# Kernel optimization log

Measured on AMD Instinct MI355X. Metric: run time of the kernel, lower is better.

The kernel has to match this reference:

```python
import jax, jax.numpy as jnp
import numpy as np

N = 8192
IN_DIM = 512
OUT_DIM = 512


def setup_inputs() -> dict:
    key = jax.random.key(0)
    kA, kX, k1, k2, k3, k4 = jax.random.split(key, 6)
    A = jax.random.uniform(kA, (N, N), dtype=jnp.float32)  # strictly positive -> nonzero triu
    X = jax.random.normal(kX, (N, IN_DIM), dtype=jnp.float32)
    s = 1.0 / np.sqrt(IN_DIM)
    W1 = jax.random.uniform(k1, (OUT_DIM, IN_DIM), minval=-s, maxval=s, dtype=jnp.float32)  # fc
    b1 = jax.random.uniform(k2, (OUT_DIM,), minval=-s, maxval=s, dtype=jnp.float32)
    W2 = jax.random.uniform(k3, (OUT_DIM, IN_DIM), minval=-s, maxval=s, dtype=jnp.float32)  # fc2
    b2 = jax.random.uniform(k4, (OUT_DIM,), minval=-s, maxval=s, dtype=jnp.float32)
    return {"A": A, "X": X, "W1": W1, "b1": b1, "W2": W2, "b2": b2}


def reference(A, X, W1, b1, W2, b2):
    n = A.shape[0]
    # strictly upper-triangular mask (diagonal=1); with uniform(0,1) fill all these
    # entries are nonzero, so torch.nonzero selects exactly them: m = n(n-1)/2 values.
    triu_mask = jnp.triu(jnp.ones((n, n), dtype=bool), k=1)
    m = n * (n - 1) // 2
    # torch.median = lower median = sorted[(m-1)//2]; pad non-triu entries with +inf
    vals = jnp.where(triu_mask, A, jnp.inf).reshape(-1)
    median_value = jnp.sort(vals)[(m - 1) // 2]
    # A[A < median] = 0
    A_thr = jnp.where(A < median_value, jnp.zeros((), A.dtype), A)
    A_norm = jax.nn.softmax(A_thr, axis=-1)
    fcX = X @ W1.T + b1    # [N, out_dim]
    fc2X = X @ W2.T + b2   # [N, out_dim]
    out = jax.nn.leaky_relu(0.1 * fc2X + 0.9 * (A_norm @ fcX), negative_slope=0.01)
    return out
```

## Files before the change

### kernel.cpp

```cpp
#include <hip/hip_runtime.h>

#define DEVI __device__ __forceinline__

typedef __attribute__((ext_vector_type(8))) short short8;
typedef __attribute__((ext_vector_type(4))) float f32x4;

static constexpr int NN = 8192;
static constexpr int DD = 512;
static constexpr unsigned LOB = 0x3EFE0000u;
static constexpr unsigned HIB = 0x3F020000u;
static constexpr long long K_RANK = 16775167LL;

static constexpr size_t WS_HIST = 0;
static constexpr size_t WS_CNT  = 1048576;
static constexpr size_t WS_MED  = 1048832;
static constexpr size_t WS_XB   = 2097152;
static constexpr size_t WS_W1B  = WS_XB  + (size_t)NN * DD * 2;
static constexpr size_t WS_W2B  = WS_W1B + (size_t)DD * DD * 2;
static constexpr size_t WS_FCXT = WS_W2B + (size_t)DD * DD * 2;
static constexpr size_t WS_FC2  = WS_FCXT + (size_t)NN * DD * 2;
static constexpr size_t WS_UP   = WS_FC2 + (size_t)NN * DD * 4;
static constexpr size_t WS_ZP   = WS_UP  + (size_t)4 * NN * DD * 2;

DEVI unsigned short f2bf(float f) {
  unsigned u = __float_as_uint(f);
  u += 0x7fffu + ((u >> 16) & 1u);
  return (unsigned short)(u >> 16);
}
DEVI float bf2f(unsigned short h) { return __uint_as_float(((unsigned)h) << 16); }
DEVI int swz(int row, int kq) { return kq ^ ((row >> 1) & 3); }

DEVI void gl_lds16(const void* g, void* l) {
  __builtin_amdgcn_global_load_lds(
      (const __attribute__((address_space(1))) unsigned*)g,
      (__attribute__((address_space(3))) unsigned*)l, 16, 0, 0);
}

#define VMCNT(n) asm volatile("s_waitcnt vmcnt(" #n ")" ::: "memory")
#define LGKM0 asm volatile("s_waitcnt lgkmcnt(0)" ::: "memory")


DEVI void convert_body(const float* __restrict__ X, const float* __restrict__ W1,
                       const float* __restrict__ W2, unsigned short* __restrict__ Xb,
                       unsigned short* __restrict__ W1b, unsigned short* __restrict__ W2b,
                       int cb, int tid) {
  const long long NX = (long long)NN * DD;
  const long long NW = (long long)DD * DD;
  const long long total4 = (NX + 2 * NW) / 4;
  for (long long q = (long long)cb * 512 + tid; q < total4; q += 65536LL) {
    long long e = q << 2;
    const float4* src; unsigned short* dst; long long off;
    if (e < NX)           { src = (const float4*)X;  dst = Xb;  off = e; }
    else if (e < NX + NW) { src = (const float4*)W1; dst = W1b; off = e - NX; }
    else                  { src = (const float4*)W2; dst = W2b; off = e - NX - NW; }
    float4 v = src[off >> 2];
    ushort4 o;
    o.x = f2bf(v.x); o.y = f2bf(v.y); o.z = f2bf(v.z); o.w = f2bf(v.w);
    *(ushort4*)(dst + off) = o;
  }
}

DEVI void hist_body(const float* __restrict__ A, unsigned* __restrict__ hist,
                    unsigned* __restrict__ below, int hb, int tid) {
  unsigned cnt = 0;
  const float4* A4 = (const float4*)A;
  for (long long q = (long long)hb * 512 + tid; q < 16777216LL; q += 458752LL) {
    long long base = q << 2;
    int row = (int)(base >> 13);
    int col = (int)(base & 8191);
    if (col + 3 <= row) continue;
    float4 v = A4[q];
    float vv[4] = {v.x, v.y, v.z, v.w};
#pragma unroll
    for (int j = 0; j < 4; ++j) {
      if (col + j > row) {
        unsigned u = __float_as_uint(vv[j]);
        if (u < LOB) cnt++;
        else if (u < HIB) atomicAdd(&hist[u - LOB], 1u);
      }
    }
  }
  for (int off = 32; off > 0; off >>= 1) cnt += __shfl_down(cnt, off);
  if ((tid & 63) == 0 && cnt) atomicAdd(below, cnt);
}

__global__ __launch_bounds__(512) void stage1_k(const float* __restrict__ A,
                                                const float* __restrict__ X,
                                                const float* __restrict__ W1,
                                                const float* __restrict__ W2,
                                                unsigned* __restrict__ hist,
                                                unsigned* __restrict__ below,
                                                unsigned short* __restrict__ Xb,
                                                unsigned short* __restrict__ W1b,
                                                unsigned short* __restrict__ W2b) {
  const int bx = blockIdx.x;
  if (bx < 128) convert_body(X, W1, W2, Xb, W1b, W2b, bx, threadIdx.x);
  else          hist_body(A, hist, below, bx - 128, threadIdx.x);
}


template <bool BROW, bool OBF>
DEVI void gemm_small_body(const unsigned short* __restrict__ Am,
                          const unsigned short* __restrict__ Bm,
                          const float* __restrict__ bias, void* __restrict__ outp,
                          int ldout, int m0, int n0, char* apB, char* btB) {
  const int tid = threadIdx.x, lane = tid & 63, w = tid >> 6;
  const int wm = w >> 2, wn = w & 3;
  const int lr = lane & 15, lq = lane >> 4;
  const int rL = lane >> 2, kq = lane & 3;
  f32x4 acc[2][4];
#pragma unroll
  for (int i = 0; i < 2; ++i)
#pragma unroll
    for (int j = 0; j < 4; ++j) acc[i][j] = (f32x4){0.f, 0.f, 0.f, 0.f};

#pragma unroll 1
  for (int kt = 0; kt < 16; ++kt) {
    const int k0 = kt * 32;
    __syncthreads();
    if (w < 4) {
      int r = w * 16 + rL;
      gl_lds16(Am + ((size_t)(m0 + r) * DD + k0 + swz(r, kq) * 8), apB + w * 1024);
    }
#pragma unroll
    for (int i = 0; i < 2; ++i) {
      int blk = w * 2 + i;
      int r = blk * 16 + rL;
      gl_lds16(Bm + ((size_t)(n0 + r) * DD + k0 + swz(r, kq) * 8), btB + blk * 1024);
    }
    __syncthreads();
    short8 a[2], b[4];
#pragma unroll
    for (int fr = 0; fr < 2; ++fr) {
      int r = wm * 32 + fr * 16 + lr;
      a[fr] = *(const short8*)(apB + r * 64 + swz(r, lq) * 16);
    }
#pragma unroll
    for (int fc = 0; fc < 4; ++fc) {
      int r = wn * 64 + fc * 16 + lr;
      b[fc] = *(const short8*)(btB + r * 64 + swz(r, lq) * 16);
    }
#pragma unroll
    for (int fr = 0; fr < 2; ++fr)
#pragma unroll
      for (int fc = 0; fc < 4; ++fc)
        acc[fr][fc] = __builtin_amdgcn_mfma_f32_16x16x32_bf16(a[fr], b[fc], acc[fr][fc], 0, 0, 0);
  }
#pragma unroll
  for (int fr = 0; fr < 2; ++fr)
#pragma unroll
    for (int fc = 0; fc < 4; ++fc)
#pragma unroll
      for (int j = 0; j < 4; ++j) {
        int row = m0 + wm * 32 + fr * 16 + lq * 4 + j;
        int col = n0 + wn * 64 + fc * 16 + lr;
        float v = acc[fr][fc][j] + (BROW ? bias[row] : bias[col]);
        if (OBF) ((unsigned short*)outp)[(size_t)row * ldout + col] = f2bf(v);
        else     ((float*)outp)[(size_t)row * ldout + col] = v;
      }
}

__global__ __launch_bounds__(512, 2) void stage2_k(const unsigned short* __restrict__ Xb,
                                                   const unsigned short* __restrict__ W1b,
                                                   const unsigned short* __restrict__ W2b,
                                                   const float* __restrict__ b1,
                                                   const float* __restrict__ b2,
                                                   unsigned short* __restrict__ fcXT,
                                                   float* __restrict__ fc2) {
  __shared__ alignas(16) char plds[20480];
  const int bx = blockIdx.x;
  if (bx < 256) {
    int m0 = ((bx >> 3) & 7) * 64;
    int n0 = ((bx & 7) | ((bx >> 6) << 3)) * 256;
    gemm_small_body<true, true>(W1b, Xb, b1, (void*)fcXT, NN, m0, n0, plds, plds + 4096);
  } else {
    int q = bx - 256;
    gemm_small_body<false, false>(Xb, W2b, b2, (void*)fc2, DD,
                                  (q >> 1) * 64, (q & 1) * 256, plds, plds + 4096);
  }
}

__global__ __launch_bounds__(1024) void select_k(const unsigned* __restrict__ hist,
                                                 const unsigned* __restrict__ below,
                                                 unsigned* __restrict__ med) {
  __shared__ unsigned ssum[1024];
  __shared__ int owner;
  __shared__ unsigned tg_s;
  const int t = threadIdx.x;
  unsigned own = 0;
  const uint4* h4 = (const uint4*)(hist + t * 256);
#pragma unroll 8
  for (int b = 0; b < 64; ++b) {
    uint4 v = h4[b];
    own += v.x + v.y + v.z + v.w;
  }
  ssum[t] = own;
  __syncthreads();
  for (int off = 1; off < 1024; off <<= 1) {
    unsigned v = (t >= off) ? ssum[t - off] : 0u;
    __syncthreads();
    ssum[t] += v;
    __syncthreads();
  }
  long long target = K_RANK - (long long)(*below);
  unsigned incl = ssum[t];
  unsigned excl = incl - own;
  if (target >= (long long)excl && target < (long long)incl) {
    owner = t;
    tg_s = (unsigned)(target - (long long)excl);
  }
  __syncthreads();
  const int to = owner;
  const unsigned tg = tg_s;
  unsigned v256 = (t < 256) ? hist[to * 256 + t] : 0u;
  __syncthreads();
  if (t < 256) ssum[t] = v256;
  __syncthreads();
  for (int off = 1; off < 256; off <<= 1) {
    unsigned v = (t < 256 && t >= off) ? ssum[t - off] : 0u;
    __syncthreads();
    if (t < 256) ssum[t] += v;
    __syncthreads();
  }
  if (t < 256) {
    unsigned incl2 = ssum[t];
    unsigned excl2 = incl2 - v256;
    if (tg >= excl2 && tg < incl2) *med = LOB + (unsigned)(to * 256 + t);
  }
}

static constexpr int LDS_A0 = 0;
static constexpr int LDS_A1 = 8192;
static constexpr int LDS_B0 = 16384;
static constexpr int LDS_B1 = 49152;

__global__ __launch_bounds__(512, 2) void main_gemm_k(const float* __restrict__ A,
                                                      const unsigned short* __restrict__ fcXT,
                                                      const unsigned* __restrict__ medp,
                                                      unsigned short* __restrict__ Up,
                                                      float* __restrict__ Zp) {
  __shared__ alignas(16) char lds[81920];
  const int tid = threadIdx.x, lane = tid & 63, w = tid >> 6;
  const int wm = w >> 2, wn = w & 3;
  const int lr = lane & 15, lq = lane >> 4;
  const int fid = blockIdx.x;
  const int xcd = fid & 7;
  const int ks = xcd >> 1;
  const int m0 = (((xcd & 1) << 5) | (fid >> 3)) << 7;
  const int kbase = ks * 2048;
  const float med = __uint_as_float(*medp);
  const int rB = lane >> 2, kqB = lane & 3;
  const int rA = tid >> 2, cqA = tid & 3;
  const float* aRow = A + (size_t)(m0 + rA) * NN;
  const int ldsAw = rA * 64 + swz(rA, cqA) * 16;

  float zacc = 0.f;
  f32x4 acc[4][8];
#pragma unroll
  for (int i = 0; i < 4; ++i)
#pragma unroll
    for (int j = 0; j < 8; ++j) acc[i][j] = (f32x4){0.f, 0.f, 0.f, 0.f};
  float4 vA00, vA01, vA10, vA11;

#define CONV8(V0, V1, DST)                                                     \
  {                                                                            \
    float vv[8] = {V0.x, V0.y, V0.z, V0.w, V1.x, V1.y, V1.z, V1.w};            \
    short8 pb;                                                                 \
    _Pragma("unroll")                                                          \
    for (int j = 0; j < 8; ++j) {                                              \
      float a_ = vv[j];                                                        \
      float p_ = (a_ < med) ? 1.0f : __expf(a_);                               \
      unsigned short h_ = f2bf(p_);                                            \
      pb[j] = (short)h_;                                                       \
      zacc += bf2f(h_);                                                        \
    }                                                                          \
    *(short8*)(DST) = pb;                                                      \
  }

  {
#pragma unroll
    for (int i = 0; i < 4; ++i) {
      int blk = w * 4 + i;
      int o = blk * 16 + rB;
      gl_lds16(fcXT + ((size_t)o * NN + kbase + swz(o, kqB) * 8), lds + LDS_B0 + blk * 1024);
    }
    const float* ap0 = aRow + kbase + cqA * 8;
    float4 t0 = *(const float4*)ap0;
    float4 t1 = *(const float4*)(ap0 + 4);
    vA00 = *(const float4*)(ap0 + 32);
    vA01 = *(const float4*)(ap0 + 36);
    CONV8(t0, t1, lds + LDS_A0 + ldsAw);
  }
  __syncthreads();

#define ITER(KT, CUR, NCUR, VAC0, VAC1, VAN0, VAN1)                            \
  {                                                                            \
    const int kt_ = (KT);                                                      \
    if (kt_ < 63) {                                                            \
      const int k1 = kbase + (kt_ + 1) * 32;                                   \
      _Pragma("unroll")                                                        \
      for (int i = 0; i < 4; ++i) {                                            \
        int blk = w * 4 + i;                                                   \
        int o = blk * 16 + rB;                                                 \
        gl_lds16(fcXT + ((size_t)o * NN + k1 + swz(o, kqB) * 8),               \
                 lds + LDS_B##NCUR + blk * 1024);                              \
      }                                                                        \
      if (kt_ < 62) {                                                          \
        const float* apf = aRow + kbase + (kt_ + 2) * 32 + cqA * 8;            \
        asm volatile("global_load_dwordx4 %0, %2, off\n\t"                     \
                     "global_load_dwordx4 %1, %2, off offset:16"               \
                     : "=&v"(VAN0), "=&v"(VAN1)                                \
                     : "v"(apf)                                                \
                     : "memory");                                              \
      }                                                                        \
    }                                                                          \
    short8 af[4], bfr[8];                                                      \
    _Pragma("unroll")                                                          \
    for (int fr = 0; fr < 4; ++fr) {                                           \
      int r = wm * 64 + fr * 16 + lr;                                          \
      af[fr] = *(const short8*)(lds + LDS_A##CUR + r * 64 + swz(r, lq) * 16);  \
    }                                                                          \
    _Pragma("unroll")                                                          \
    for (int fc = 0; fc < 8; ++fc) {                                           \
      int o = wn * 128 + fc * 16 + lr;                                         \
      bfr[fc] = *(const short8*)(lds + LDS_B##CUR + o * 64 + swz(o, lq) * 16); \
    }                                                                          \
    __builtin_amdgcn_s_setprio(1);                                             \
    _Pragma("unroll")                                                          \
    for (int fr = 0; fr < 4; ++fr)                                             \
      _Pragma("unroll")                                                        \
      for (int fc = 0; fc < 8; ++fc)                                           \
        acc[fr][fc] = __builtin_amdgcn_mfma_f32_16x16x32_bf16(af[fr], bfr[fc], \
                                                              acc[fr][fc], 0, 0, 0); \
    __builtin_amdgcn_s_setprio(0);                                             \
    if (kt_ < 63) {                                                            \
      if (kt_ < 62) { VMCNT(6); } else { VMCNT(4); }                           \
      __builtin_amdgcn_sched_barrier(0);                                       \
      CONV8(VAC0, VAC1, lds + LDS_A##NCUR + ldsAw);                            \
      if (kt_ < 62) { VMCNT(2); } else { VMCNT(0); }                           \
      LGKM0;                                                                   \
      __builtin_amdgcn_s_barrier();                                            \
    }                                                                          \
  }

#pragma unroll 1
  for (int t2 = 0; t2 < 32; ++t2) {
    ITER(2 * t2,     0, 1, vA00, vA01, vA10, vA11);
    ITER(2 * t2 + 1, 1, 0, vA10, vA11, vA00, vA01);
  }
#undef ITER
#undef CONV8

  zacc += __shfl_xor(zacc, 1);
  zacc += __shfl_xor(zacc, 2);
  if ((lane & 3) == 0) Zp[(size_t)ks * NN + m0 + rA] = zacc;
#pragma unroll
  for (int fr = 0; fr < 4; ++fr)
#pragma unroll
    for (int fc = 0; fc < 8; ++fc)
#pragma unroll
      for (int j = 0; j < 4; ++j) {
        int row = m0 + wm * 64 + fr * 16 + lq * 4 + j;
        int col = wn * 128 + fc * 16 + lr;
        Up[((size_t)ks << 22) + ((size_t)row << 9) + col] = f2bf(acc[fr][fc][j]);
      }
}

__global__ __launch_bounds__(256) void reduce_k(const unsigned short* __restrict__ Up,
                                                const float* __restrict__ Zp,
                                                const float* __restrict__ fc2,
                                                float* __restrict__ out) {
  long long t = (long long)blockIdx.x * blockDim.x + threadIdx.x;
  if (t >= (long long)NN * DD / 8) return;
  long long base = t << 3;
  int row = (int)(base >> 9);
  float Z = Zp[row] + Zp[NN + row] + Zp[2 * NN + row] + Zp[3 * NN + row];
  float inv = 0.9f / Z;
  float s[8] = {0, 0, 0, 0, 0, 0, 0, 0};
#pragma unroll
  for (int sp = 0; sp < 4; ++sp) {
    const uint4 u = *(const uint4*)(Up + ((long long)sp << 22) + base);
    const unsigned uu[4] = {u.x, u.y, u.z, u.w};
#pragma unroll
    for (int j = 0; j < 4; ++j) {
      s[2 * j]     += __uint_as_float(uu[j] << 16);
      s[2 * j + 1] += __uint_as_float(uu[j] & 0xffff0000u);
    }
  }
  float4 fa = *(const float4*)(fc2 + base);
  float4 fb = *(const float4*)(fc2 + base + 4);
  float fv[8] = {fa.x, fa.y, fa.z, fa.w, fb.x, fb.y, fb.z, fb.w};
  float o[8];
#pragma unroll
  for (int j = 0; j < 8; ++j) {
    float v = 0.1f * fv[j] + inv * s[j];
    o[j] = v >= 0.f ? v : 0.01f * v;
  }
  *(float4*)(out + base)     = (float4){o[0], o[1], o[2], o[3]};
  *(float4*)(out + base + 4) = (float4){o[4], o[5], o[6], o[7]};
}

extern "C" void kernel_launch(void* const* d_in, const int* in_sizes, int n_in,
                              void* d_out, int out_size, void* d_ws, size_t ws_size,
                              hipStream_t stream) {
  const float* A  = (const float*)d_in[0];
  const float* X  = (const float*)d_in[1];
  const float* W1 = (const float*)d_in[2];
  const float* b1 = (const float*)d_in[3];
  const float* W2 = (const float*)d_in[4];
  const float* b2 = (const float*)d_in[5];
  char* ws = (char*)d_ws;
  unsigned* hist = (unsigned*)(ws + WS_HIST);
  unsigned* cnt  = (unsigned*)(ws + WS_CNT);
  unsigned* med  = (unsigned*)(ws + WS_MED);
  unsigned short* Xb   = (unsigned short*)(ws + WS_XB);
  unsigned short* W1b  = (unsigned short*)(ws + WS_W1B);
  unsigned short* W2b  = (unsigned short*)(ws + WS_W2B);
  unsigned short* fcXT = (unsigned short*)(ws + WS_FCXT);
  float* fc2           = (float*)(ws + WS_FC2);
  unsigned short* Upp  = (unsigned short*)(ws + WS_UP);
  float* Zp            = (float*)(ws + WS_ZP);

  hipMemsetAsync(ws, 0, 1048576 + 512, stream);
  hipLaunchKernelGGL(stage1_k, dim3(1024), dim3(512), 0, stream,
                     A, X, W1, W2, hist, cnt, Xb, W1b, W2b);
  hipLaunchKernelGGL(stage2_k, dim3(512), dim3(512), 0, stream,
                     Xb, W1b, W2b, b1, b2, fcXT, fc2);
  hipLaunchKernelGGL(select_k, dim3(1), dim3(1024), 0, stream, hist, cnt, med);
  hipLaunchKernelGGL(main_gemm_k, dim3(256), dim3(512), 0, stream, A, fcXT, med, Upp, Zp);
  hipLaunchKernelGGL(reduce_k, dim3(2048), dim3(256), 0, stream, Upp, Zp, fc2, (float*)d_out);
}
```

Baseline: 268.4 us.

## Deepen fcXT LDS pipeline to four buffers with prefetch distance two

```diff
diff --git a/kernel.cpp b/kernel.cpp
--- a/kernel.cpp
+++ b/kernel.cpp
@@ -233,13 +233,15 @@
 static constexpr int LDS_A1 = 8192;
 static constexpr int LDS_B0 = 16384;
 static constexpr int LDS_B1 = 49152;
+static constexpr int LDS_B2 = 81920;
+static constexpr int LDS_B3 = 114688;
 
 __global__ __launch_bounds__(512, 2) void main_gemm_k(const float* __restrict__ A,
                                                       const unsigned short* __restrict__ fcXT,
                                                       const unsigned* __restrict__ medp,
                                                       unsigned short* __restrict__ Up,
                                                       float* __restrict__ Zp) {
-  __shared__ alignas(16) char lds[81920];
+  __shared__ alignas(16) char lds[147456];
   const int tid = threadIdx.x, lane = tid & 63, w = tid >> 6;
   const int wm = w >> 2, wn = w & 3;
   const int lr = lane & 15, lq = lane >> 4;
@@ -278,52 +280,61 @@
   }
 
   {
+    const float* ap0 = aRow + kbase + cqA * 8;
+    float4 t0 = *(const float4*)ap0;
+    float4 t1 = *(const float4*)(ap0 + 4);
+    CONV8(t0, t1, lds + LDS_A0 + ldsAw);
+    const float* ap1 = aRow + kbase + 32 + cqA * 8;
+    asm volatile("global_load_dwordx4 %0, %2, off\n\t"
+                 "global_load_dwordx4 %1, %2, off offset:16"
+                 : "=&v"(vA00), "=&v"(vA01) : "v"(ap1) : "memory");
 #pragma unroll
     for (int i = 0; i < 4; ++i) {
       int blk = w * 4 + i;
       int o = blk * 16 + rB;
       gl_lds16(fcXT + ((size_t)o * NN + kbase + swz(o, kqB) * 8), lds + LDS_B0 + blk * 1024);
     }
-    const float* ap0 = aRow + kbase + cqA * 8;
-    float4 t0 = *(const float4*)ap0;
-    float4 t1 = *(const float4*)(ap0 + 4);
-    vA00 = *(const float4*)(ap0 + 32);
-    vA01 = *(const float4*)(ap0 + 36);
-    CONV8(t0, t1, lds + LDS_A0 + ldsAw);
-  }
-  __syncthreads();
-
-#define ITER(KT, CUR, NCUR, VAC0, VAC1, VAN0, VAN1)                            \
+#pragma unroll
+    for (int i = 0; i < 4; ++i) {
+      int blk = w * 4 + i;
+      int o = blk * 16 + rB;
+      gl_lds16(fcXT + ((size_t)o * NN + kbase + 32 + swz(o, kqB) * 8), lds + LDS_B1 + blk * 1024);
+    }
+    VMCNT(4);
+    __builtin_amdgcn_sched_barrier(0);
+    LGKM0;
+    __builtin_amdgcn_s_barrier();
+  }
+
+#define ITER(KT, ACUR, ANXT, BCUR, BISS, VAC0, VAC1, VAN0, VAN1)               \
   {                                                                            \
     const int kt_ = (KT);                                                      \
-    if (kt_ < 63) {                                                            \
-      const int k1 = kbase + (kt_ + 1) * 32;                                   \
+    if (kt_ < 62) {                                                            \
+      const float* apf = aRow + kbase + (kt_ + 2) * 32 + cqA * 8;              \
+      asm volatile("global_load_dwordx4 %0, %2, off\n\t"                       \
+                   "global_load_dwordx4 %1, %2, off offset:16"                 \
+                   : "=&v"(VAN0), "=&v"(VAN1)                                  \
+                   : "v"(apf)                                                  \
+                   : "memory");                                                \
+      const int k2 = kbase + (kt_ + 2) * 32;                                   \
       _Pragma("unroll")                                                        \
       for (int i = 0; i < 4; ++i) {                                            \
         int blk = w * 4 + i;                                                   \
         int o = blk * 16 + rB;                                                 \
-        gl_lds16(fcXT + ((size_t)o * NN + k1 + swz(o, kqB) * 8),               \
-                 lds + LDS_B##NCUR + blk * 1024);                              \
-      }                                                                        \
-      if (kt_ < 62) {                                                          \
-        const float* apf = aRow + kbase + (kt_ + 2) * 32 + cqA * 8;            \
-        asm volatile("global_load_dwordx4 %0, %2, off\n\t"                     \
-                     "global_load_dwordx4 %1, %2, off offset:16"               \
-                     : "=&v"(VAN0), "=&v"(VAN1)                                \
-                     : "v"(apf)                                                \
-                     : "memory");                                              \
+        gl_lds16(fcXT + ((size_t)o * NN + k2 + swz(o, kqB) * 8),               \
+                 lds + LDS_B##BISS + blk * 1024);                              \
       }                                                                        \
     }                                                                          \
     short8 af[4], bfr[8];                                                      \
     _Pragma("unroll")                                                          \
     for (int fr = 0; fr < 4; ++fr) {                                           \
       int r = wm * 64 + fr * 16 + lr;                                          \
-      af[fr] = *(const short8*)(lds + LDS_A##CUR + r * 64 + swz(r, lq) * 16);  \
+      af[fr] = *(const short8*)(lds + LDS_A##ACUR + r * 64 + swz(r, lq) * 16); \
     }                                                                          \
     _Pragma("unroll")                                                          \
     for (int fc = 0; fc < 8; ++fc) {                                           \
       int o = wn * 128 + fc * 16 + lr;                                         \
-      bfr[fc] = *(const short8*)(lds + LDS_B##CUR + o * 64 + swz(o, lq) * 16); \
+      bfr[fc] = *(const short8*)(lds + LDS_B##BCUR + o * 64 + swz(o, lq) * 16);\
     }                                                                          \
     __builtin_amdgcn_s_setprio(1);                                             \
     _Pragma("unroll")                                                          \
@@ -334,19 +345,21 @@
                                                               acc[fr][fc], 0, 0, 0); \
     __builtin_amdgcn_s_setprio(0);                                             \
     if (kt_ < 63) {                                                            \
-      if (kt_ < 62) { VMCNT(6); } else { VMCNT(4); }                           \
+      if (kt_ < 62) { VMCNT(10); } else { VMCNT(4); }                          \
       __builtin_amdgcn_sched_barrier(0);                                       \
-      CONV8(VAC0, VAC1, lds + LDS_A##NCUR + ldsAw);                            \
-      if (kt_ < 62) { VMCNT(2); } else { VMCNT(0); }                           \
+      CONV8(VAC0, VAC1, lds + LDS_A##ANXT + ldsAw);                            \
+      if (kt_ < 62) { VMCNT(6); } else { VMCNT(0); }                           \
       LGKM0;                                                                   \
       __builtin_amdgcn_s_barrier();                                            \
     }                                                                          \
   }
 
 #pragma unroll 1
-  for (int t2 = 0; t2 < 32; ++t2) {
-    ITER(2 * t2,     0, 1, vA00, vA01, vA10, vA11);
-    ITER(2 * t2 + 1, 1, 0, vA10, vA11, vA00, vA01);
+  for (int t4 = 0; t4 < 16; ++t4) {
+    ITER(4 * t4 + 0, 0, 1, 0, 2, vA00, vA01, vA10, vA11);
+    ITER(4 * t4 + 1, 1, 0, 1, 3, vA10, vA11, vA00, vA01);
+    ITER(4 * t4 + 2, 0, 1, 2, 0, vA00, vA01, vA10, vA11);
+    ITER(4 * t4 + 3, 1, 0, 3, 1, vA10, vA11, vA00, vA01);
   }
 #undef ITER
 #undef CONV8
```

Result: slower. 370.7 us (+38.1%).

## Double main GEMM block to 1024 threads with smaller per-wave tiles

Applied to the files above, without the earlier changes.

```diff
diff --git a/kernel.cpp b/kernel.cpp
--- a/kernel.cpp
+++ b/kernel.cpp
@@ -3,6 +3,7 @@
 #define DEVI __device__ __forceinline__
 
 typedef __attribute__((ext_vector_type(8))) short short8;
+typedef __attribute__((ext_vector_type(4))) short short4v;
 typedef __attribute__((ext_vector_type(4))) float f32x4;
 
 static constexpr int NN = 8192;
@@ -234,14 +235,14 @@
 static constexpr int LDS_B0 = 16384;
 static constexpr int LDS_B1 = 49152;
 
-__global__ __launch_bounds__(512, 2) void main_gemm_k(const float* __restrict__ A,
-                                                      const unsigned short* __restrict__ fcXT,
-                                                      const unsigned* __restrict__ medp,
-                                                      unsigned short* __restrict__ Up,
-                                                      float* __restrict__ Zp) {
+__global__ __launch_bounds__(1024, 4) void main_gemm_k(const float* __restrict__ A,
+                                                       const unsigned short* __restrict__ fcXT,
+                                                       const unsigned* __restrict__ medp,
+                                                       unsigned short* __restrict__ Up,
+                                                       float* __restrict__ Zp) {
   __shared__ alignas(16) char lds[81920];
   const int tid = threadIdx.x, lane = tid & 63, w = tid >> 6;
-  const int wm = w >> 2, wn = w & 3;
+  const int wm = w >> 3, wn = w & 7;
   const int lr = lane & 15, lq = lane >> 4;
   const int fid = blockIdx.x;
   const int xcd = fid & 7;
@@ -250,94 +251,88 @@
   const int kbase = ks * 2048;
   const float med = __uint_as_float(*medp);
   const int rB = lane >> 2, kqB = lane & 3;
-  const int rA = tid >> 2, cqA = tid & 3;
+  const int rA = tid >> 3, cqA = tid & 7;
   const float* aRow = A + (size_t)(m0 + rA) * NN;
-  const int ldsAw = rA * 64 + swz(rA, cqA) * 16;
+  const int ldsAw = rA * 64 + swz(rA, cqA >> 1) * 16 + (cqA & 1) * 8;
 
   float zacc = 0.f;
-  f32x4 acc[4][8];
+  f32x4 acc[4][4];
 #pragma unroll
   for (int i = 0; i < 4; ++i)
 #pragma unroll
-    for (int j = 0; j < 8; ++j) acc[i][j] = (f32x4){0.f, 0.f, 0.f, 0.f};
-  float4 vA00, vA01, vA10, vA11;
-
-#define CONV8(V0, V1, DST)                                                     \
+    for (int j = 0; j < 4; ++j) acc[i][j] = (f32x4){0.f, 0.f, 0.f, 0.f};
+  float4 vA0, vA1;
+
+#define CONV4(V, DST)                                                          \
   {                                                                            \
-    float vv[8] = {V0.x, V0.y, V0.z, V0.w, V1.x, V1.y, V1.z, V1.w};            \
-    short8 pb;                                                                 \
+    float vv[4] = {V.x, V.y, V.z, V.w};                                        \
+    short4v pb;                                                                \
     _Pragma("unroll")                                                          \
-    for (int j = 0; j < 8; ++j) {                                              \
+    for (int j = 0; j < 4; ++j) {                                              \
       float a_ = vv[j];                                                        \
       float p_ = (a_ < med) ? 1.0f : __expf(a_);                               \
       unsigned short h_ = f2bf(p_);                                            \
       pb[j] = (short)h_;                                                       \
       zacc += bf2f(h_);                                                        \
     }                                                                          \
-    *(short8*)(DST) = pb;                                                      \
+    *(short4v*)(DST) = pb;                                                     \
   }
 
   {
 #pragma unroll
-    for (int i = 0; i < 4; ++i) {
-      int blk = w * 4 + i;
+    for (int i = 0; i < 2; ++i) {
+      int blk = w * 2 + i;
       int o = blk * 16 + rB;
       gl_lds16(fcXT + ((size_t)o * NN + kbase + swz(o, kqB) * 8), lds + LDS_B0 + blk * 1024);
     }
-    const float* ap0 = aRow + kbase + cqA * 8;
-    float4 t0 = *(const float4*)ap0;
-    float4 t1 = *(const float4*)(ap0 + 4);
-    vA00 = *(const float4*)(ap0 + 32);
-    vA01 = *(const float4*)(ap0 + 36);
-    CONV8(t0, t1, lds + LDS_A0 + ldsAw);
+    float4 t0 = *(const float4*)(aRow + kbase + cqA * 4);
+    vA0 = *(const float4*)(aRow + kbase + 32 + cqA * 4);
+    CONV4(t0, lds + LDS_A0 + ldsAw);
   }
   __syncthreads();
 
-#define ITER(KT, CUR, NCUR, VAC0, VAC1, VAN0, VAN1)                            \
+#define ITER(KT, CUR, NCUR, VAC, VAN)                                          \
   {                                                                            \
     const int kt_ = (KT);                                                      \
     if (kt_ < 63) {                                                            \
       const int k1 = kbase + (kt_ + 1) * 32;                                   \
       _Pragma("unroll")                                                        \
-      for (int i = 0; i < 4; ++i) {                                            \
-        int blk = w * 4 + i;                                                   \
+      for (int i = 0; i < 2; ++i) {                                            \
+        int blk = w * 2 + i;                                                   \
         int o = blk * 16 + rB;                                                 \
         gl_lds16(fcXT + ((size_t)o * NN + k1 + swz(o, kqB) * 8),               \
                  lds + LDS_B##NCUR + blk * 1024);                              \
       }                                                                        \
       if (kt_ < 62) {                                                          \
-        const float* apf = aRow + kbase + (kt_ + 2) * 32 + cqA * 8;            \
-        asm volatile("global_load_dwordx4 %0, %2, off\n\t"                     \
-                     "global_load_dwordx4 %1, %2, off offset:16"               \
-                     : "=&v"(VAN0), "=&v"(VAN1)                                \
-                     : "v"(apf)                                                \
-                     : "memory");                                              \
+        const float* apf = aRow + kbase + (kt_ + 2) * 32 + cqA * 4;            \
+        asm volatile("global_load_dwordx4 %0, %1, off"                         \
+                     : "=&v"(VAN) : "v"(apf) : "memory");                      \
       }                                                                        \
     }                                                                          \
-    short8 af[4], bfr[8];                                                      \
+    short8 af[4], bfr[4];                                                      \
     _Pragma("unroll")                                                          \
     for (int fr = 0; fr < 4; ++fr) {                                           \
       int r = wm * 64 + fr * 16 + lr;                                          \
       af[fr] = *(const short8*)(lds + LDS_A##CUR + r * 64 + swz(r, lq) * 16);  \
     }                                                                          \
     _Pragma("unroll")                                                          \
-    for (int fc = 0; fc < 8; ++fc) {                                           \
-      int o = wn * 128 + fc * 16 + lr;                                         \
+    for (int fc = 0; fc < 4; ++fc) {                                           \
+      int o = wn * 64 + fc * 16 + lr;                                          \
       bfr[fc] = *(const short8*)(lds + LDS_B##CUR + o * 64 + swz(o, lq) * 16); \
     }                                                                          \
     __builtin_amdgcn_s_setprio(1);                                             \
     _Pragma("unroll")                                                          \
     for (int fr = 0; fr < 4; ++fr)                                             \
       _Pragma("unroll")                                                        \
-      for (int fc = 0; fc < 8; ++fc)                                           \
+      for (int fc = 0; fc < 4; ++fc)                                           \
         acc[fr][fc] = __builtin_amdgcn_mfma_f32_16x16x32_bf16(af[fr], bfr[fc], \
                                                               acc[fr][fc], 0, 0, 0); \
     __builtin_amdgcn_s_setprio(0);                                             \
     if (kt_ < 63) {                                                            \
-      if (kt_ < 62) { VMCNT(6); } else { VMCNT(4); }                           \
+      if (kt_ < 62) { VMCNT(3); } else { VMCNT(2); }                           \
       __builtin_amdgcn_sched_barrier(0);                                       \
-      CONV8(VAC0, VAC1, lds + LDS_A##NCUR + ldsAw);                            \
-      if (kt_ < 62) { VMCNT(2); } else { VMCNT(0); }                           \
+      CONV4(VAC, lds + LDS_A##NCUR + ldsAw);                                   \
+      if (kt_ < 62) { VMCNT(1); } else { VMCNT(0); }                           \
       LGKM0;                                                                   \
       __builtin_amdgcn_s_barrier();                                            \
     }                                                                          \
@@ -345,23 +340,24 @@
 
 #pragma unroll 1
   for (int t2 = 0; t2 < 32; ++t2) {
-    ITER(2 * t2,     0, 1, vA00, vA01, vA10, vA11);
-    ITER(2 * t2 + 1, 1, 0, vA10, vA11, vA00, vA01);
+    ITER(2 * t2,     0, 1, vA0, vA1);
+    ITER(2 * t2 + 1, 1, 0, vA1, vA0);
   }
 #undef ITER
-#undef CONV8
+#undef CONV4
 
   zacc += __shfl_xor(zacc, 1);
   zacc += __shfl_xor(zacc, 2);
-  if ((lane & 3) == 0) Zp[(size_t)ks * NN + m0 + rA] = zacc;
+  zacc += __shfl_xor(zacc, 4);
+  if ((tid & 7) == 0) Zp[(size_t)ks * NN + m0 + rA] = zacc;
 #pragma unroll
   for (int fr = 0; fr < 4; ++fr)
 #pragma unroll
-    for (int fc = 0; fc < 8; ++fc)
+    for (int fc = 0; fc < 4; ++fc)
 #pragma unroll
       for (int j = 0; j < 4; ++j) {
         int row = m0 + wm * 64 + fr * 16 + lq * 4 + j;
-        int col = wn * 128 + fc * 16 + lr;
+        int col = wn * 64 + fc * 16 + lr;
         Up[((size_t)ks << 22) + ((size_t)row << 9) + col] = f2bf(acc[fr][fc][j]);
       }
 }
@@ -427,6 +423,6 @@
   hipLaunchKernelGGL(stage2_k, dim3(512), dim3(512), 0, stream,
                      Xb, W1b, W2b, b1, b2, fcXT, fc2);
   hipLaunchKernelGGL(select_k, dim3(1), dim3(1024), 0, stream, hist, cnt, med);
-  hipLaunchKernelGGL(main_gemm_k, dim3(256), dim3(512), 0, stream, A, fcXT, med, Upp, Zp);
+  hipLaunchKernelGGL(main_gemm_k, dim3(256), dim3(1024), 0, stream, A, fcXT, med, Upp, Zp);
   hipLaunchKernelGGL(reduce_k, dim3(2048), dim3(256), 0, stream, Upp, Zp, fc2, (float*)d_out);
 }
```

Measured after the change: 280.0 us. 1.04x slower.
